# Kernel tuning notes

Measured on AMD Instinct MI355X. Metric: run time of the kernel, lower is better.

## Reference

```python
import jax, jax.numpy as jnp
import numpy as np

EMB = 128
HID = 4 * 32  # 4*hidden_dim = 128
N_NODES = 100000
N_EDGES = 800000


def setup_inputs() -> dict:
    key = jax.random.key(0)
    k1, k2, k3, k4 = jax.random.split(key, 4)
    node_emb = jax.random.normal(k1, (N_NODES, EMB), dtype=jnp.float32)
    edge_index = jax.random.randint(k2, (2, N_EDGES), 0, N_NODES, dtype=jnp.int64)
    # xavier_uniform for Linear weights, zeros bias; LayerNorm gamma=1, beta=0
    lim1 = float(np.sqrt(6.0 / (2 * EMB + HID)))
    W1 = jax.random.uniform(k3, (2 * EMB, HID), minval=-lim1, maxval=lim1, dtype=jnp.float32)
    b1 = jnp.zeros((HID,), dtype=jnp.float32)
    ln_g = jnp.ones((HID,), dtype=jnp.float32)
    ln_b = jnp.zeros((HID,), dtype=jnp.float32)
    lim2 = float(np.sqrt(6.0 / (HID + 1)))
    W2 = jax.random.uniform(k4, (HID, 1), minval=-lim2, maxval=lim2, dtype=jnp.float32)
    b2 = jnp.zeros((1,), dtype=jnp.float32)
    return {"node_emb": node_emb, "edge_index": edge_index,
            "W1": W1, "b1": b1, "ln_g": ln_g, "ln_b": ln_b, "W2": W2, "b2": b2}


def reference(node_emb, edge_index, W1, b1, ln_g, ln_b, W2, b2):
    src, dst = edge_index[0], edge_index[1]
    # gather + concat: [E, 2*EMB]
    edge_emb = jnp.concatenate([node_emb[src], node_emb[dst]], axis=1)
    h = edge_emb @ W1 + b1  # [E, HID]
    # LayerNorm over last dim (eps=1e-5, torch default)
    mu = jnp.mean(h, axis=-1, keepdims=True)
    var = jnp.var(h, axis=-1, keepdims=True)
    h = (h - mu) * jax.lax.rsqrt(var + 1e-5) * ln_g + ln_b
    h = jax.nn.relu(h)  # Dropout is identity in eval mode
    w = jax.nn.sigmoid(h @ W2 + b2)  # [E, 1]
    w = jnp.nan_to_num(w, nan=0.5)
    return w
```

## Files before the change

### kernel.cpp

```cpp
#include <hip/hip_runtime.h>
#include <hip/hip_bf16.h>
#include <math.h>

#define EMB 128
#define HID 128
#define NCOL 256

typedef __attribute__((ext_vector_type(8))) short short8v;
typedef __attribute__((ext_vector_type(4))) float f32x4;
typedef __attribute__((ext_vector_type(8))) unsigned short ushort8v;

__device__ __forceinline__ short f2bf(float f) {
    union { float f; unsigned int u; } v; v.f = f;
    unsigned int r = (v.u + 0x7FFFu + ((v.u >> 16) & 1u)) >> 16;
    return (short)r;
}
__device__ __forceinline__ float bf2f(unsigned short u) {
    return __uint_as_float(((unsigned int)u) << 16);
}

__global__ __launch_bounds__(256) void w_prep(
    const float* __restrict__ W1, unsigned short* __restrict__ Wt)
{
    int idx = blockIdx.x * 256 + threadIdx.x;
    int c = idx >> 7;
    int k = idx & 127;
    float v = W1[(size_t)(k + ((c >> 7) << 7)) * HID + (c & 127)];
    Wt[idx] = (unsigned short)f2bf(v);
}

__global__ __launch_bounds__(256) void proj_mfma(
    const float* __restrict__ A,
    const unsigned short* __restrict__ Wt,
    unsigned short* __restrict__ P,
    int N, int nTiles)
{
    const int w    = threadIdx.x >> 6;
    const int lane = threadIdx.x & 63;
    const int l16  = lane & 15;
    const int lk   = lane >> 4;

    short8v bfrag[4][4];
#pragma unroll
    for (int cf = 0; cf < 4; ++cf)
#pragma unroll
        for (int ks = 0; ks < 4; ++ks) {
            int c = 64 * w + 16 * cf + l16;
            int k = 32 * ks + 8 * lk;
            bfrag[cf][ks] = *(const short8v*)(Wt + (size_t)c * EMB + k);
        }

    for (int t = blockIdx.x; t < nTiles; t += gridDim.x) {
        const int m0 = t * 64;
        f32x4 acc[4][4];
#pragma unroll
        for (int rf = 0; rf < 4; ++rf)
#pragma unroll
            for (int cf = 0; cf < 4; ++cf) acc[rf][cf] = (f32x4)0.0f;

#pragma unroll
        for (int ks = 0; ks < 4; ++ks) {
#pragma unroll
            for (int rf = 0; rf < 4; ++rf) {
                int row = m0 + 16 * rf + l16;
                row = row < N ? row : N - 1;
                const float* ap = A + (size_t)row * EMB + 32 * ks + 8 * lk;
                float4 a0 = *(const float4*)ap;
                float4 a1 = *(const float4*)(ap + 4);
                short8v af = { f2bf(a0.x), f2bf(a0.y), f2bf(a0.z), f2bf(a0.w),
                               f2bf(a1.x), f2bf(a1.y), f2bf(a1.z), f2bf(a1.w) };
#pragma unroll
                for (int cf = 0; cf < 4; ++cf)
                    acc[rf][cf] = __builtin_amdgcn_mfma_f32_16x16x32_bf16(
                        af, bfrag[cf][ks], acc[rf][cf], 0, 0, 0);
            }
        }
#pragma unroll
        for (int rf = 0; rf < 4; ++rf) {
#pragma unroll
            for (int cf = 0; cf < 4; ++cf) {
                int col = 64 * w + 16 * cf + l16;
                int rb  = m0 + 16 * rf + 4 * lk;
#pragma unroll
                for (int r = 0; r < 4; ++r) {
                    int row = rb + r;
                    if (row < N)
                        P[(size_t)row * NCOL + col] = (unsigned short)f2bf(acc[rf][cf][r]);
                }
            }
        }
    }
}

__global__ __launch_bounds__(256) void edge_kernel(
    const unsigned short* __restrict__ P,
    const int* __restrict__ ei,
    const float* __restrict__ b1,
    const float* __restrict__ lng,
    const float* __restrict__ lnb,
    const float* __restrict__ W2,
    const float* __restrict__ b2,
    float* __restrict__ out, int E)
{
    const int l16 = threadIdx.x & 15;
    const int c0  = l16 * 8;

    float vb1[8], vg[8], vbt[8], vw2[8];
#pragma unroll
    for (int i = 0; i < 8; i += 4) {
        *(float4*)&vb1[i] = *(const float4*)(b1  + c0 + i);
        *(float4*)&vg[i]  = *(const float4*)(lng + c0 + i);
        *(float4*)&vbt[i] = *(const float4*)(lnb + c0 + i);
        *(float4*)&vw2[i] = *(const float4*)(W2  + c0 + i);
    }
    const float bias2 = b2[0];

    int slot   = blockIdx.x * (blockDim.x >> 4) + (threadIdx.x >> 4);
    int nslots = gridDim.x * (blockDim.x >> 4);

    for (int e = slot; e < E; e += nslots) {
        int src = ei[e];
        int dst = ei[E + e];
        ushort8v ps = *(const ushort8v*)(P + (size_t)src * NCOL + c0);
        ushort8v pd = *(const ushort8v*)(P + (size_t)dst * NCOL + HID + c0);

        float h[8];
        float s = 0.0f, sq = 0.0f;
#pragma unroll
        for (int i = 0; i < 8; ++i) {
            h[i] = bf2f(ps[i]) + bf2f(pd[i]) + vb1[i];
            s  += h[i];
            sq += h[i] * h[i];
        }
#pragma unroll
        for (int m = 8; m >= 1; m >>= 1) {
            s  += __shfl_xor(s,  m, 16);
            sq += __shfl_xor(sq, m, 16);
        }
        float mu  = s * (1.0f / HID);
        float var = sq * (1.0f / HID) - mu * mu;
        float r   = rsqrtf(var + 1e-5f);

        float z = 0.0f;
#pragma unroll
        for (int i = 0; i < 8; ++i) {
            float y = fmaxf(fmaf((h[i] - mu) * r, vg[i], vbt[i]), 0.0f);
            z = fmaf(y, vw2[i], z);
        }
#pragma unroll
        for (int m = 8; m >= 1; m >>= 1) z += __shfl_xor(z, m, 16);

        if (l16 == 0) {
            float zz = z + bias2;
            float wv = 1.0f / (1.0f + expf(-zz));
            if (wv != wv) wv = 0.5f;
            out[e] = wv;
        }
    }
}

__global__ __launch_bounds__(256) void fused_kernel(
    const float* __restrict__ X,
    const int* __restrict__ ei,
    const float* __restrict__ W1,
    const float* __restrict__ b1,
    const float* __restrict__ lng,
    const float* __restrict__ lnb,
    const float* __restrict__ W2,
    const float* __restrict__ b2,
    float* __restrict__ out, int E)
{
    const int lane = threadIdx.x & 31;
    const int c0   = lane * 4;
    const float4 vb1 = *(const float4*)(b1  + c0);
    const float4 vg  = *(const float4*)(lng + c0);
    const float4 vbt = *(const float4*)(lnb + c0);
    const float4 vw2 = *(const float4*)(W2  + c0);
    const float bias2 = b2[0];

    int slot   = blockIdx.x * (blockDim.x >> 5) + (threadIdx.x >> 5);
    int nslots = gridDim.x * (blockDim.x >> 5);

    for (int e = slot; e < E; e += nslots) {
        int src = ei[e];
        int dst = ei[E + e];
        const float* xs = X + (size_t)src * EMB;
        const float* xd = X + (size_t)dst * EMB;
        float h0 = vb1.x, h1 = vb1.y, h2 = vb1.z, h3 = vb1.w;
        for (int k = 0; k < EMB; ++k) {
            float a  = xs[k];
            float4 w = *(const float4*)(W1 + (size_t)k * HID + c0);
            h0 = fmaf(a, w.x, h0); h1 = fmaf(a, w.y, h1);
            h2 = fmaf(a, w.z, h2); h3 = fmaf(a, w.w, h3);
        }
        for (int k = 0; k < EMB; ++k) {
            float a  = xd[k];
            float4 w = *(const float4*)(W1 + (size_t)(EMB + k) * HID + c0);
            h0 = fmaf(a, w.x, h0); h1 = fmaf(a, w.y, h1);
            h2 = fmaf(a, w.z, h2); h3 = fmaf(a, w.w, h3);
        }
        float s  = h0 + h1 + h2 + h3;
        float sq = h0 * h0 + h1 * h1 + h2 * h2 + h3 * h3;
#pragma unroll
        for (int m = 16; m >= 1; m >>= 1) {
            s  += __shfl_xor(s,  m, 32);
            sq += __shfl_xor(sq, m, 32);
        }
        float mu  = s * (1.0f / HID);
        float var = sq * (1.0f / HID) - mu * mu;
        float r   = rsqrtf(var + 1e-5f);
        float y0 = fmaxf(fmaf((h0 - mu) * r, vg.x, vbt.x), 0.0f);
        float y1 = fmaxf(fmaf((h1 - mu) * r, vg.y, vbt.y), 0.0f);
        float y2 = fmaxf(fmaf((h2 - mu) * r, vg.z, vbt.z), 0.0f);
        float y3 = fmaxf(fmaf((h3 - mu) * r, vg.w, vbt.w), 0.0f);
        float z = y0 * vw2.x + y1 * vw2.y + y2 * vw2.z + y3 * vw2.w;
#pragma unroll
        for (int m = 16; m >= 1; m >>= 1) z += __shfl_xor(z, m, 32);
        if (lane == 0) {
            float zz = z + bias2;
            float wv = 1.0f / (1.0f + expf(-zz));
            if (wv != wv) wv = 0.5f;
            out[e] = wv;
        }
    }
}

extern "C" void kernel_launch(void* const* d_in, const int* in_sizes, int n_in,
                              void* d_out, int out_size, void* d_ws, size_t ws_size,
                              hipStream_t stream) {
    const float* node_emb = (const float*)d_in[0];
    const int*   ei       = (const int*)d_in[1];
    const float* W1       = (const float*)d_in[2];
    const float* b1       = (const float*)d_in[3];
    const float* lng      = (const float*)d_in[4];
    const float* lnb      = (const float*)d_in[5];
    const float* W2       = (const float*)d_in[6];
    const float* b2       = (const float*)d_in[7];
    float* out = (float*)d_out;

    const int N = in_sizes[0] / EMB;
    const int E = in_sizes[1] / 2;

    const size_t pBytes = (size_t)N * NCOL * sizeof(unsigned short);
    const size_t need   = pBytes + (size_t)NCOL * EMB * sizeof(unsigned short);

    if (ws_size >= need) {
        unsigned short* P  = (unsigned short*)d_ws;
        unsigned short* Wt = (unsigned short*)((char*)d_ws + pBytes);

        w_prep<<<(NCOL * EMB) / 256, 256, 0, stream>>>(W1, Wt);

        int nTiles = (N + 63) / 64;
        int gridP  = (nTiles + 1) / 2;
        proj_mfma<<<gridP, 256, 0, stream>>>(node_emb, Wt, P, N, nTiles);

        edge_kernel<<<2048, 256, 0, stream>>>(P, ei, b1, lng, lnb, W2, b2, out, E);
    } else {
        fused_kernel<<<2048, 256, 0, stream>>>(node_emb, ei, W1, b1, lng, lnb,
                                               W2, b2, out, E);
    }
}
```

Baseline: 204.1 us.

## Transpose projection MFMA so each lane stores contiguous bf16 outputs per node

The projection kernel now swaps the MFMA operands, using W as the A operand and 16 nodes as the B operand, so each lane holds four consecutive output columns for one node. It writes them as packed 8-byte stores instead of scattered 2-byte stores. Tiles shrink to 16 nodes with a grid capped at 2048, which cuts per-tile register use but reloads nothing extra because W fragments stay resident. The edge kernel unpacks bf16 pairs from uint4 loads with shift/mask and folds the LayerNorm mean subtraction into an FMA.

```diff
diff --git a/kernel.cpp b/kernel.cpp
--- a/kernel.cpp
+++ b/kernel.cpp
@@ -8,15 +8,11 @@
 
 typedef __attribute__((ext_vector_type(8))) short short8v;
 typedef __attribute__((ext_vector_type(4))) float f32x4;
-typedef __attribute__((ext_vector_type(8))) unsigned short ushort8v;
-
-__device__ __forceinline__ short f2bf(float f) {
+
+__device__ __forceinline__ unsigned short f2bf(float f) {
     union { float f; unsigned int u; } v; v.f = f;
     unsigned int r = (v.u + 0x7FFFu + ((v.u >> 16) & 1u)) >> 16;
-    return (short)r;
-}
-__device__ __forceinline__ float bf2f(unsigned short u) {
-    return __uint_as_float(((unsigned int)u) << 16);
+    return (unsigned short)r;
 }
 
 __global__ __launch_bounds__(256) void w_prep(
@@ -26,7 +22,7 @@
     int c = idx >> 7;
     int k = idx & 127;
     float v = W1[(size_t)(k + ((c >> 7) << 7)) * HID + (c & 127)];
-    Wt[idx] = (unsigned short)f2bf(v);
+    Wt[idx] = f2bf(v);
 }
 
 __global__ __launch_bounds__(256) void proj_mfma(
@@ -40,53 +36,52 @@
     const int l16  = lane & 15;
     const int lk   = lane >> 4;
 
-    short8v bfrag[4][4];
+    short8v afrag[4][4];
 #pragma unroll
     for (int cf = 0; cf < 4; ++cf)
 #pragma unroll
         for (int ks = 0; ks < 4; ++ks) {
             int c = 64 * w + 16 * cf + l16;
-            int k = 32 * ks + 8 * lk;
-            bfrag[cf][ks] = *(const short8v*)(Wt + (size_t)c * EMB + k);
+            afrag[cf][ks] = *(const short8v*)(Wt + (size_t)c * EMB + 32 * ks + 8 * lk);
         }
 
     for (int t = blockIdx.x; t < nTiles; t += gridDim.x) {
-        const int m0 = t * 64;
-        f32x4 acc[4][4];
-#pragma unroll
-        for (int rf = 0; rf < 4; ++rf)
-#pragma unroll
-            for (int cf = 0; cf < 4; ++cf) acc[rf][cf] = (f32x4)0.0f;
-
+        const int n0   = t * 16;
+        int node = n0 + l16;
+        int nc   = node < N ? node : N - 1;
+        const float* ap = A + (size_t)nc * EMB + 8 * lk;
+
+        short8v bf[4];
 #pragma unroll
         for (int ks = 0; ks < 4; ++ks) {
-#pragma unroll
-            for (int rf = 0; rf < 4; ++rf) {
-                int row = m0 + 16 * rf + l16;
-                row = row < N ? row : N - 1;
-                const float* ap = A + (size_t)row * EMB + 32 * ks + 8 * lk;
-                float4 a0 = *(const float4*)ap;
-                float4 a1 = *(const float4*)(ap + 4);
-                short8v af = { f2bf(a0.x), f2bf(a0.y), f2bf(a0.z), f2bf(a0.w),
-                               f2bf(a1.x), f2bf(a1.y), f2bf(a1.z), f2bf(a1.w) };
-#pragma unroll
-                for (int cf = 0; cf < 4; ++cf)
-                    acc[rf][cf] = __builtin_amdgcn_mfma_f32_16x16x32_bf16(
-                        af, bfrag[cf][ks], acc[rf][cf], 0, 0, 0);
-            }
-        }
-#pragma unroll
-        for (int rf = 0; rf < 4; ++rf) {
+            float4 a0 = *(const float4*)(ap + 32 * ks);
+            float4 a1 = *(const float4*)(ap + 32 * ks + 4);
+            short8v f = { (short)f2bf(a0.x), (short)f2bf(a0.y), (short)f2bf(a0.z), (short)f2bf(a0.w),
+                          (short)f2bf(a1.x), (short)f2bf(a1.y), (short)f2bf(a1.z), (short)f2bf(a1.w) };
+            bf[ks] = f;
+        }
+
+        f32x4 acc[4];
+#pragma unroll
+        for (int cf = 0; cf < 4; ++cf) acc[cf] = (f32x4)0.0f;
+
+#pragma unroll
+        for (int ks = 0; ks < 4; ++ks)
+#pragma unroll
+            for (int cf = 0; cf < 4; ++cf)
+                acc[cf] = __builtin_amdgcn_mfma_f32_16x16x32_bf16(
+                    afrag[cf][ks], bf[ks], acc[cf], 0, 0, 0);
+
+        if (node < N) {
+            unsigned short* prow = P + (size_t)node * NCOL;
 #pragma unroll
             for (int cf = 0; cf < 4; ++cf) {
-                int col = 64 * w + 16 * cf + l16;
-                int rb  = m0 + 16 * rf + 4 * lk;
-#pragma unroll
-                for (int r = 0; r < 4; ++r) {
-                    int row = rb + r;
-                    if (row < N)
-                        P[(size_t)row * NCOL + col] = (unsigned short)f2bf(acc[rf][cf][r]);
-                }
+                unsigned int u0 = (unsigned int)f2bf(acc[cf][0]) |
+                                  ((unsigned int)f2bf(acc[cf][1]) << 16);
+                unsigned int u1 = (unsigned int)f2bf(acc[cf][2]) |
+                                  ((unsigned int)f2bf(acc[cf][3]) << 16);
+                uint2 v = make_uint2(u0, u1);
+                *(uint2*)(prow + 64 * w + 16 * cf + 4 * lk) = v;
             }
         }
     }
@@ -121,16 +116,28 @@
     for (int e = slot; e < E; e += nslots) {
         int src = ei[e];
         int dst = ei[E + e];
-        ushort8v ps = *(const ushort8v*)(P + (size_t)src * NCOL + c0);
-        ushort8v pd = *(const ushort8v*)(P + (size_t)dst * NCOL + HID + c0);
+        uint4 us = *(const uint4*)(P + (size_t)src * NCOL + c0);
+        uint4 ud = *(const uint4*)(P + (size_t)dst * NCOL + HID + c0);
 
         float h[8];
+        {
+            unsigned int uu[4] = {us.x, us.y, us.z, us.w};
+            unsigned int dd[4] = {ud.x, ud.y, ud.z, ud.w};
+#pragma unroll
+            for (int j = 0; j < 4; ++j) {
+                float a0 = __uint_as_float(uu[j] << 16);
+                float a1 = __uint_as_float(uu[j] & 0xFFFF0000u);
+                float d0 = __uint_as_float(dd[j] << 16);
+                float d1 = __uint_as_float(dd[j] & 0xFFFF0000u);
+                h[2 * j]     = a0 + d0 + vb1[2 * j];
+                h[2 * j + 1] = a1 + d1 + vb1[2 * j + 1];
+            }
+        }
         float s = 0.0f, sq = 0.0f;
 #pragma unroll
         for (int i = 0; i < 8; ++i) {
-            h[i] = bf2f(ps[i]) + bf2f(pd[i]) + vb1[i];
-            s  += h[i];
-            sq += h[i] * h[i];
+            s += h[i];
+            sq = fmaf(h[i], h[i], sq);
         }
 #pragma unroll
         for (int m = 8; m >= 1; m >>= 1) {
@@ -140,11 +147,14 @@
         float mu  = s * (1.0f / HID);
         float var = sq * (1.0f / HID) - mu * mu;
         float r   = rsqrtf(var + 1e-5f);
+        float nmr = -mu * r;
 
         float z = 0.0f;
 #pragma unroll
         for (int i = 0; i < 8; ++i) {
-            float y = fmaxf(fmaf((h[i] - mu) * r, vg[i], vbt[i]), 0.0f);
+            float t = fmaf(h[i], r, nmr);
+            float y = fmaf(t, vg[i], vbt[i]);
+            y = fmaxf(y, 0.0f);
             z = fmaf(y, vw2[i], z);
         }
 #pragma unroll
@@ -250,8 +260,8 @@
 
         w_prep<<<(NCOL * EMB) / 256, 256, 0, stream>>>(W1, Wt);
 
-        int nTiles = (N + 63) / 64;
-        int gridP  = (nTiles + 1) / 2;
+        int nTiles = (N + 15) / 16;
+        int gridP  = nTiles < 2048 ? nTiles : 2048;
         proj_mfma<<<gridP, 256, 0, stream>>>(node_emb, Wt, P, N, nTiles);
 
         edge_kernel<<<2048, 256, 0, stream>>>(P, ei, b1, lng, lnb, W2, b2, out, E);
```

Result: faster. 198.0 us (-3.0%).
